# Kernel tuning notes

Hardware: AMD Instinct MI355X
Metric: run time of the kernel (lower is better)

Reference implementation:

```python
import jax, jax.numpy as jnp
import numpy as np

SCALE = 0.08838834764831845  # 1/sqrt(128)


def setup_inputs() -> dict:
    key = jax.random.key(0)
    k1, k2, k3, k4, k5 = jax.random.split(key, 5)
    B, H, KVH, D = 32, 32, 8, 128
    NUM_BLOCKS, BLOCK_SIZE, MAX_BLOCKS = 1200, 128, 32
    return {
        "query": jax.random.normal(k1, (B, H, D), dtype=jnp.float32),
        "key_cache": jax.random.normal(k2, (NUM_BLOCKS, BLOCK_SIZE, KVH, D), dtype=jnp.float32),
        "value_cache": jax.random.normal(k3, (NUM_BLOCKS, BLOCK_SIZE, KVH, D), dtype=jnp.float32),
        "block_tables": jax.random.randint(k4, (B, MAX_BLOCKS), 0, NUM_BLOCKS, dtype=jnp.int32),
        "context_lens": jax.random.randint(k5, (B,), 1, MAX_BLOCKS * BLOCK_SIZE, dtype=jnp.int32),
    }


def reference(query, key_cache, value_cache, block_tables, context_lens):
    # Paged attention v1 decode (single query token per sequence, GQA).
    B, H, D = query.shape
    NB = block_tables.shape[1]
    BS, KVH = key_cache.shape[1], key_cache.shape[2]
    G = H // KVH  # queries per kv head
    S = NB * BS   # padded kv length

    # Gather cache blocks per sequence: [B, NB, BS, KVH, D] -> [B, KVH, S, D]
    keys = key_cache[block_tables].transpose(0, 3, 1, 2, 4).reshape(B, KVH, S, D)
    vals = value_cache[block_tables].transpose(0, 3, 1, 2, 4).reshape(B, KVH, S, D)

    q = (query * SCALE).reshape(B, KVH, G, D)
    scores = jnp.einsum('bkgd,bksd->bkgs', q, keys)  # [B, KVH, G, S]

    # Mask positions beyond context length with dtype-min (as masked_fill in torch).
    pos = jnp.arange(S, dtype=jnp.int32)
    invalid = pos[None, :] >= context_lens[:, None]  # [B, S]
    scores = jnp.where(invalid[:, None, None, :], jnp.finfo(scores.dtype).min, scores)

    w = jax.nn.softmax(scores, axis=-1)
    out = jnp.einsum('bkgs,bksd->bkgd', w, vals).reshape(B, H, D)
    return out
```

## Files before the change

### kernel.cpp

```cpp
#include <hip/hip_runtime.h>

#define SCALE 0.08838834764831845f

constexpr int B_    = 32;
constexpr int H_    = 32;
constexpr int KVH_  = 8;
constexpr int G_    = 4;
constexpr int D_    = 128;
constexpr int BS_   = 128;
constexpr int MAXB_ = 32;
constexpr int NSPLIT = 8;
constexpr int CHUNK  = 4096 / NSPLIT;
constexpr int NBLK_PER_CHUNK = CHUNK / BS_;

__global__ __launch_bounds__(256) void attn_partial(
    const float* __restrict__ q,
    const float* __restrict__ kc,
    const float* __restrict__ vc,
    const int*   __restrict__ bt,
    const int*   __restrict__ ctxl,
    float*       __restrict__ part_o,
    float*       __restrict__ part_ml)
{
    const int bid   = blockIdx.x;
    const int split = bid & (NSPLIT - 1);
    const int kv    = (bid >> 3) & (KVH_ - 1);
    const int b     = bid >> 6;
    const int tid   = threadIdx.x;

    const int ctx   = ctxl[b];
    const int start = split * CHUNK;
    int clen = ctx - start;
    if (clen > CHUNK) clen = CHUNK;

    const int mlbase = ((b * KVH_ + kv) * NSPLIT + split) * G_ * 2;
    if (clen <= 0) {
        if (tid < G_) {
            part_ml[mlbase + tid * 2 + 0] = -__builtin_inff();
            part_ml[mlbase + tid * 2 + 1] = 0.f;
        }
        return;
    }

    __shared__ float q_s[G_ * D_];
    __shared__ float logit[G_][CHUNK];
    __shared__ float red[8 * G_ * D_];
    __shared__ int   blk_s[NBLK_PER_CHUNK];
    __shared__ float red_m[4][G_];
    __shared__ float red_l[4][G_];

    for (int i = tid; i < G_ * D_; i += 256) {
        int g = i >> 7, d = i & (D_ - 1);
        q_s[i] = q[((size_t)b * H_ + kv * G_ + g) * D_ + d] * SCALE;
    }
    if (tid < NBLK_PER_CHUNK)
        blk_s[tid] = bt[b * MAXB_ + split * NBLK_PER_CHUNK + tid];
    __syncthreads();

    {
        const int ln16 = tid & 15;
        const int cl   = tid >> 4;

        float4 qr[G_][2];
#pragma unroll
        for (int g = 0; g < G_; g++) {
            const float4* qp = (const float4*)(q_s + g * D_);
            qr[g][0] = qp[ln16];
            qr[g][1] = qp[ln16 + 16];
        }

#pragma unroll 2
        for (int p = cl; p < clen; p += 16) {
            const int blk = blk_s[p >> 7];
            const int off = p & (BS_ - 1);
            const float4* kp =
                (const float4*)(kc + ((((size_t)blk * BS_ + off) * KVH_ + kv) << 7))
                + ln16;
            float4 ka = kp[0];
            float4 kb = kp[16];
            float s[G_];
#pragma unroll
            for (int g = 0; g < G_; g++) {
                s[g] = ka.x * qr[g][0].x + ka.y * qr[g][0].y +
                       ka.z * qr[g][0].z + ka.w * qr[g][0].w +
                       kb.x * qr[g][1].x + kb.y * qr[g][1].y +
                       kb.z * qr[g][1].z + kb.w * qr[g][1].w;
            }
#pragma unroll
            for (int m = 8; m >= 1; m >>= 1) {
#pragma unroll
                for (int g = 0; g < G_; g++)
                    s[g] += __shfl_xor(s[g], m, 64);
            }
            if (ln16 == 0) {
#pragma unroll
                for (int g = 0; g < G_; g++) logit[g][p] = s[g];
            }
        }
    }
    __syncthreads();

    float ml[G_];
#pragma unroll
    for (int g = 0; g < G_; g++) ml[g] = -__builtin_inff();
    for (int i = tid; i < clen; i += 256) {
#pragma unroll
        for (int g = 0; g < G_; g++) ml[g] = fmaxf(ml[g], logit[g][i]);
    }
#pragma unroll
    for (int m = 32; m >= 1; m >>= 1) {
#pragma unroll
        for (int g = 0; g < G_; g++)
            ml[g] = fmaxf(ml[g], __shfl_xor(ml[g], m, 64));
    }
    if ((tid & 63) == 0) {
#pragma unroll
        for (int g = 0; g < G_; g++) red_m[tid >> 6][g] = ml[g];
    }
    __syncthreads();
    float M[G_];
#pragma unroll
    for (int g = 0; g < G_; g++)
        M[g] = fmaxf(fmaxf(red_m[0][g], red_m[1][g]),
                     fmaxf(red_m[2][g], red_m[3][g]));

    float ll[G_] = {0.f, 0.f, 0.f, 0.f};
    for (int i = tid; i < clen; i += 256) {
#pragma unroll
        for (int g = 0; g < G_; g++) {
            float pv = __expf(logit[g][i] - M[g]);
            logit[g][i] = pv;
            ll[g] += pv;
        }
    }
#pragma unroll
    for (int m = 32; m >= 1; m >>= 1) {
#pragma unroll
        for (int g = 0; g < G_; g++) ll[g] += __shfl_xor(ll[g], m, 64);
    }
    if ((tid & 63) == 0) {
#pragma unroll
        for (int g = 0; g < G_; g++) red_l[tid >> 6][g] = ll[g];
    }
    __syncthreads();
    float L[G_];
#pragma unroll
    for (int g = 0; g < G_; g++)
        L[g] = red_l[0][g] + red_l[1][g] + red_l[2][g] + red_l[3][g];

    const int lane = tid & 31;
    const int grp  = tid >> 5;

    float4 acc[G_] = {};
#pragma unroll 2
    for (int i = grp; i < clen; i += 8) {
        const int blk = blk_s[i >> 7];
        const int off = i & (BS_ - 1);
        const float4* vp =
            (const float4*)(vc + ((((size_t)blk * BS_ + off) * KVH_ + kv) << 7));
        float4 v4 = vp[lane];
#pragma unroll
        for (int g = 0; g < G_; g++) {
            float w = logit[g][i];
            acc[g].x += w * v4.x; acc[g].y += w * v4.y;
            acc[g].z += w * v4.z; acc[g].w += w * v4.w;
        }
    }
    float4* red4 = (float4*)red;
#pragma unroll
    for (int g = 0; g < G_; g++)
        red4[(grp * G_ + g) * 32 + lane] = acc[g];
    __syncthreads();

    const size_t obase = (size_t)((b * KVH_ + kv) * NSPLIT + split) * (G_ * D_);
    for (int e = tid; e < G_ * D_; e += 256) {
        float sum = 0.f;
#pragma unroll
        for (int p = 0; p < 8; p++) sum += red[p * (G_ * D_) + e];
        part_o[obase + e] = sum;
    }
    if (tid == 0) {
#pragma unroll
        for (int g = 0; g < G_; g++) {
            part_ml[mlbase + g * 2 + 0] = M[g];
            part_ml[mlbase + g * 2 + 1] = L[g];
        }
    }
}

__global__ __launch_bounds__(256) void attn_reduce(
    const float* __restrict__ part_o,
    const float* __restrict__ part_ml,
    float*       __restrict__ out)
{
    const int bid = blockIdx.x;
    const int tid = threadIdx.x;

    __shared__ float sc[G_][NSPLIT];
    __shared__ float Ls[G_];

    if (tid < G_) {
        float m = -__builtin_inff();
        float lv[NSPLIT], mv[NSPLIT];
#pragma unroll
        for (int s = 0; s < NSPLIT; s++) {
            mv[s] = part_ml[((size_t)bid * NSPLIT + s) * G_ * 2 + tid * 2 + 0];
            lv[s] = part_ml[((size_t)bid * NSPLIT + s) * G_ * 2 + tid * 2 + 1];
            if (lv[s] > 0.f) m = fmaxf(m, mv[s]);
        }
        float L = 0.f;
#pragma unroll
        for (int s = 0; s < NSPLIT; s++) {
            float f = (lv[s] > 0.f) ? __expf(mv[s] - m) : 0.f;
            sc[tid][s] = f;
            L += f * lv[s];
        }
        Ls[tid] = L;
    }
    __syncthreads();

    for (int e = tid; e < G_ * D_; e += 256) {
        int g = e >> 7;
        float a = 0.f;
#pragma unroll
        for (int s = 0; s < NSPLIT; s++) {
            float f = sc[g][s];
            if (f != 0.f)
                a += f * part_o[((size_t)bid * NSPLIT + s) * (G_ * D_) + e];
        }
        out[(size_t)bid * (G_ * D_) + e] = a / Ls[g];
    }
}

extern "C" void kernel_launch(void* const* d_in, const int* in_sizes, int n_in,
                              void* d_out, int out_size, void* d_ws, size_t ws_size,
                              hipStream_t stream) {
    const float* q   = (const float*)d_in[0];
    const float* kc  = (const float*)d_in[1];
    const float* vc  = (const float*)d_in[2];
    const int*   bt  = (const int*)d_in[3];
    const int*   ctx = (const int*)d_in[4];
    float* out = (float*)d_out;

    float* part_o  = (float*)d_ws;
    float* part_ml = part_o + (size_t)B_ * KVH_ * NSPLIT * G_ * D_;

    attn_partial<<<B_ * KVH_ * NSPLIT, 256, 0, stream>>>(q, kc, vc, bt, ctx,
                                                         part_o, part_ml);
    attn_reduce<<<B_ * KVH_, 256, 0, stream>>>(part_o, part_ml, out);
}
```

Measured before the change: 1.060 ms.

## Process all KV heads per block over contiguous 64-token chunks with 64 splits

```diff
diff --git a/kernel.cpp b/kernel.cpp
--- a/kernel.cpp
+++ b/kernel.cpp
@@ -9,9 +9,9 @@
 constexpr int D_    = 128;
 constexpr int BS_   = 128;
 constexpr int MAXB_ = 32;
-constexpr int NSPLIT = 8;
+constexpr int NSPLIT = 64;
 constexpr int CHUNK  = 4096 / NSPLIT;
-constexpr int NBLK_PER_CHUNK = CHUNK / BS_;
+constexpr int LPAD   = 36;
 
 __global__ __launch_bounds__(256) void attn_partial(
     const float* __restrict__ q,
@@ -24,168 +24,108 @@
 {
     const int bid   = blockIdx.x;
     const int split = bid & (NSPLIT - 1);
-    const int kv    = (bid >> 3) & (KVH_ - 1);
     const int b     = bid >> 6;
     const int tid   = threadIdx.x;
 
-    const int ctx   = ctxl[b];
-    const int start = split * CHUNK;
-    int clen = ctx - start;
+    const int ctx = ctxl[b];
+    int clen = ctx - split * CHUNK;
     if (clen > CHUNK) clen = CHUNK;
-
-    const int mlbase = ((b * KVH_ + kv) * NSPLIT + split) * G_ * 2;
     if (clen <= 0) {
-        if (tid < G_) {
-            part_ml[mlbase + tid * 2 + 0] = -__builtin_inff();
-            part_ml[mlbase + tid * 2 + 1] = 0.f;
+        if (tid < KVH_ * G_) {
+            const int kv = tid >> 2, g = tid & 3;
+            const size_t mb =
+                ((size_t)(b * KVH_ + kv) * NSPLIT + split) * (G_ * 2) + g * 2;
+            part_ml[mb + 0] = -__builtin_inff();
+            part_ml[mb + 1] = 0.f;
         }
         return;
     }
 
-    __shared__ float q_s[G_ * D_];
-    __shared__ float logit[G_][CHUNK];
-    __shared__ float red[8 * G_ * D_];
-    __shared__ int   blk_s[NBLK_PER_CHUNK];
-    __shared__ float red_m[4][G_];
-    __shared__ float red_l[4][G_];
+    __shared__ __align__(16) float logit2[CHUNK][LPAD];
 
-    for (int i = tid; i < G_ * D_; i += 256) {
-        int g = i >> 7, d = i & (D_ - 1);
-        q_s[i] = q[((size_t)b * H_ + kv * G_ + g) * D_ + d] * SCALE;
+    const int hw  = tid >> 5;
+    const int l32 = tid & 31;
+
+    const int blk  = bt[b * MAXB_ + (split >> 1)];
+    const int poff = (split & 1) * CHUNK;
+    const float* kbase =
+        kc + (((size_t)blk * BS_ + poff) * KVH_ + hw) * D_ + l32 * 4;
+
+    float4 qf[G_];
+#pragma unroll
+    for (int g = 0; g < G_; g++) {
+        qf[g] = *(const float4*)(q + ((size_t)b * H_ + hw * G_ + g) * D_ + l32 * 4);
+        qf[g].x *= SCALE; qf[g].y *= SCALE; qf[g].z *= SCALE; qf[g].w *= SCALE;
     }
-    if (tid < NBLK_PER_CHUNK)
-        blk_s[tid] = bt[b * MAXB_ + split * NBLK_PER_CHUNK + tid];
+
+#pragma unroll 2
+    for (int p = 0; p < clen; ++p) {
+        const float4 k4 = *(const float4*)(kbase + (size_t)p * (KVH_ * D_));
+        float s0 = k4.x*qf[0].x + k4.y*qf[0].y + k4.z*qf[0].z + k4.w*qf[0].w;
+        float s1 = k4.x*qf[1].x + k4.y*qf[1].y + k4.z*qf[1].z + k4.w*qf[1].w;
+        float s2 = k4.x*qf[2].x + k4.y*qf[2].y + k4.z*qf[2].z + k4.w*qf[2].w;
+        float s3 = k4.x*qf[3].x + k4.y*qf[3].y + k4.z*qf[3].z + k4.w*qf[3].w;
+#pragma unroll
+        for (int m = 4; m <= 16; m <<= 1) {
+            s0 += __shfl_xor(s0, m, 64);
+            s1 += __shfl_xor(s1, m, 64);
+            s2 += __shfl_xor(s2, m, 64);
+            s3 += __shfl_xor(s3, m, 64);
+        }
+        const bool o1 = (l32 & 1) != 0, o2 = (l32 & 2) != 0;
+        float a01 = o1 ? s0 : s1;  float r01 = __shfl_xor(a01, 1, 64);
+        float uA  = (o1 ? s1 : s0) + r01;
+        float a23 = o1 ? s2 : s3;  float r23 = __shfl_xor(a23, 1, 64);
+        float uB  = (o1 ? s3 : s2) + r23;
+        float v   = o2 ? uA : uB;  float rv  = __shfl_xor(v, 2, 64);
+        float fin = (o2 ? uB : uA) + rv;
+        if (l32 < 4) logit2[p][hw * G_ + l32] = fin;
+    }
     __syncthreads();
 
     {
-        const int ln16 = tid & 15;
-        const int cl   = tid >> 4;
-
-        float4 qr[G_][2];
+        const int h = tid >> 3, ln8 = tid & 7;
+        float m = -__builtin_inff();
+        for (int i = ln8; i < clen; i += 8) m = fmaxf(m, logit2[i][h]);
 #pragma unroll
-        for (int g = 0; g < G_; g++) {
-            const float4* qp = (const float4*)(q_s + g * D_);
-            qr[g][0] = qp[ln16];
-            qr[g][1] = qp[ln16 + 16];
+        for (int mk = 4; mk >= 1; mk >>= 1)
+            m = fmaxf(m, __shfl_xor(m, mk, 64));
+        float l = 0.f;
+        for (int i = ln8; i < clen; i += 8) {
+            float pv = __expf(logit2[i][h] - m);
+            logit2[i][h] = pv;
+            l += pv;
         }
-
-#pragma unroll 2
-        for (int p = cl; p < clen; p += 16) {
-            const int blk = blk_s[p >> 7];
-            const int off = p & (BS_ - 1);
-            const float4* kp =
-                (const float4*)(kc + ((((size_t)blk * BS_ + off) * KVH_ + kv) << 7))
-                + ln16;
-            float4 ka = kp[0];
-            float4 kb = kp[16];
-            float s[G_];
 #pragma unroll
-            for (int g = 0; g < G_; g++) {
-                s[g] = ka.x * qr[g][0].x + ka.y * qr[g][0].y +
-                       ka.z * qr[g][0].z + ka.w * qr[g][0].w +
-                       kb.x * qr[g][1].x + kb.y * qr[g][1].y +
-                       kb.z * qr[g][1].z + kb.w * qr[g][1].w;
-            }
-#pragma unroll
-            for (int m = 8; m >= 1; m >>= 1) {
-#pragma unroll
-                for (int g = 0; g < G_; g++)
-                    s[g] += __shfl_xor(s[g], m, 64);
-            }
-            if (ln16 == 0) {
-#pragma unroll
-                for (int g = 0; g < G_; g++) logit[g][p] = s[g];
-            }
+        for (int mk = 4; mk >= 1; mk >>= 1) l += __shfl_xor(l, mk, 64);
+        if (ln8 == 0) {
+            const size_t mb =
+                ((size_t)(b * KVH_ + (h >> 2)) * NSPLIT + split) * (G_ * 2) +
+                (h & 3) * 2;
+            part_ml[mb + 0] = m;
+            part_ml[mb + 1] = l;
         }
     }
     __syncthreads();
 
-    float ml[G_];
-#pragma unroll
-    for (int g = 0; g < G_; g++) ml[g] = -__builtin_inff();
-    for (int i = tid; i < clen; i += 256) {
-#pragma unroll
-        for (int g = 0; g < G_; g++) ml[g] = fmaxf(ml[g], logit[g][i]);
+    const float* vbase =
+        vc + (((size_t)blk * BS_ + poff) * KVH_ + hw) * D_ + l32 * 4;
+    float4 a0 = {0,0,0,0}, a1 = {0,0,0,0}, a2 = {0,0,0,0}, a3 = {0,0,0,0};
+#pragma unroll 4
+    for (int p = 0; p < clen; ++p) {
+        const float4 v4 = *(const float4*)(vbase + (size_t)p * (KVH_ * D_));
+        const float4 w4 = *(const float4*)(&logit2[p][hw * G_]);
+        a0.x += w4.x * v4.x; a0.y += w4.x * v4.y; a0.z += w4.x * v4.z; a0.w += w4.x * v4.w;
+        a1.x += w4.y * v4.x; a1.y += w4.y * v4.y; a1.z += w4.y * v4.z; a1.w += w4.y * v4.w;
+        a2.x += w4.z * v4.x; a2.y += w4.z * v4.y; a2.z += w4.z * v4.z; a2.w += w4.z * v4.w;
+        a3.x += w4.w * v4.x; a3.y += w4.w * v4.y; a3.z += w4.w * v4.z; a3.w += w4.w * v4.w;
     }
-#pragma unroll
-    for (int m = 32; m >= 1; m >>= 1) {
-#pragma unroll
-        for (int g = 0; g < G_; g++)
-            ml[g] = fmaxf(ml[g], __shfl_xor(ml[g], m, 64));
-    }
-    if ((tid & 63) == 0) {
-#pragma unroll
-        for (int g = 0; g < G_; g++) red_m[tid >> 6][g] = ml[g];
-    }
-    __syncthreads();
-    float M[G_];
-#pragma unroll
-    for (int g = 0; g < G_; g++)
-        M[g] = fmaxf(fmaxf(red_m[0][g], red_m[1][g]),
-                     fmaxf(red_m[2][g], red_m[3][g]));
-
-    float ll[G_] = {0.f, 0.f, 0.f, 0.f};
-    for (int i = tid; i < clen; i += 256) {
-#pragma unroll
-        for (int g = 0; g < G_; g++) {
-            float pv = __expf(logit[g][i] - M[g]);
-            logit[g][i] = pv;
-            ll[g] += pv;
-        }
-    }
-#pragma unroll
-    for (int m = 32; m >= 1; m >>= 1) {
-#pragma unroll
-        for (int g = 0; g < G_; g++) ll[g] += __shfl_xor(ll[g], m, 64);
-    }
-    if ((tid & 63) == 0) {
-#pragma unroll
-        for (int g = 0; g < G_; g++) red_l[tid >> 6][g] = ll[g];
-    }
-    __syncthreads();
-    float L[G_];
-#pragma unroll
-    for (int g = 0; g < G_; g++)
-        L[g] = red_l[0][g] + red_l[1][g] + red_l[2][g] + red_l[3][g];
-
-    const int lane = tid & 31;
-    const int grp  = tid >> 5;
-
-    float4 acc[G_] = {};
-#pragma unroll 2
-    for (int i = grp; i < clen; i += 8) {
-        const int blk = blk_s[i >> 7];
-        const int off = i & (BS_ - 1);
-        const float4* vp =
-            (const float4*)(vc + ((((size_t)blk * BS_ + off) * KVH_ + kv) << 7));
-        float4 v4 = vp[lane];
-#pragma unroll
-        for (int g = 0; g < G_; g++) {
-            float w = logit[g][i];
-            acc[g].x += w * v4.x; acc[g].y += w * v4.y;
-            acc[g].z += w * v4.z; acc[g].w += w * v4.w;
-        }
-    }
-    float4* red4 = (float4*)red;
-#pragma unroll
-    for (int g = 0; g < G_; g++)
-        red4[(grp * G_ + g) * 32 + lane] = acc[g];
-    __syncthreads();
-
-    const size_t obase = (size_t)((b * KVH_ + kv) * NSPLIT + split) * (G_ * D_);
-    for (int e = tid; e < G_ * D_; e += 256) {
-        float sum = 0.f;
-#pragma unroll
-        for (int p = 0; p < 8; p++) sum += red[p * (G_ * D_) + e];
-        part_o[obase + e] = sum;
-    }
-    if (tid == 0) {
-#pragma unroll
-        for (int g = 0; g < G_; g++) {
-            part_ml[mlbase + g * 2 + 0] = M[g];
-            part_ml[mlbase + g * 2 + 1] = L[g];
-        }
-    }
+    const size_t ob =
+        ((size_t)(b * KVH_ + hw) * NSPLIT + split) * (G_ * D_) + l32 * 4;
+    *(float4*)(part_o + ob + 0 * D_) = a0;
+    *(float4*)(part_o + ob + 1 * D_) = a1;
+    *(float4*)(part_o + ob + 2 * D_) = a2;
+    *(float4*)(part_o + ob + 3 * D_) = a3;
 }
 
 __global__ __launch_bounds__(256) void attn_reduce(
@@ -199,32 +139,30 @@
     __shared__ float sc[G_][NSPLIT];
     __shared__ float Ls[G_];
 
-    if (tid < G_) {
-        float m = -__builtin_inff();
-        float lv[NSPLIT], mv[NSPLIT];
+    {
+        const int g = tid >> 6, s = tid & 63;
+        const size_t base = ((size_t)bid * NSPLIT + s) * (G_ * 2) + g * 2;
+        const float mv = part_ml[base + 0];
+        const float lv = part_ml[base + 1];
+        float key = (lv > 0.f) ? mv : -__builtin_inff();
 #pragma unroll
-        for (int s = 0; s < NSPLIT; s++) {
-            mv[s] = part_ml[((size_t)bid * NSPLIT + s) * G_ * 2 + tid * 2 + 0];
-            lv[s] = part_ml[((size_t)bid * NSPLIT + s) * G_ * 2 + tid * 2 + 1];
-            if (lv[s] > 0.f) m = fmaxf(m, mv[s]);
-        }
-        float L = 0.f;
+        for (int mk = 32; mk >= 1; mk >>= 1)
+            key = fmaxf(key, __shfl_xor(key, mk, 64));
+        const float f = (lv > 0.f) ? __expf(mv - key) : 0.f;
+        sc[g][s] = f;
+        float fl = f * lv;
 #pragma unroll
-        for (int s = 0; s < NSPLIT; s++) {
-            float f = (lv[s] > 0.f) ? __expf(mv[s] - m) : 0.f;
-            sc[tid][s] = f;
-            L += f * lv[s];
-        }
-        Ls[tid] = L;
+        for (int mk = 32; mk >= 1; mk >>= 1) fl += __shfl_xor(fl, mk, 64);
+        if (s == 0) Ls[g] = fl;
     }
     __syncthreads();
 
     for (int e = tid; e < G_ * D_; e += 256) {
-        int g = e >> 7;
+        const int g = e >> 7;
         float a = 0.f;
-#pragma unroll
+#pragma unroll 4
         for (int s = 0; s < NSPLIT; s++) {
-            float f = sc[g][s];
+            const float f = sc[g][s];
             if (f != 0.f)
                 a += f * part_o[((size_t)bid * NSPLIT + s) * (G_ * D_) + e];
         }
@@ -245,7 +183,7 @@
     float* part_o  = (float*)d_ws;
     float* part_ml = part_o + (size_t)B_ * KVH_ * NSPLIT * G_ * D_;
 
-    attn_partial<<<B_ * KVH_ * NSPLIT, 256, 0, stream>>>(q, kc, vc, bt, ctx,
-                                                         part_o, part_ml);
+    attn_partial<<<B_ * NSPLIT, 256, 0, stream>>>(q, kc, vc, bt, ctx,
+                                                  part_o, part_ml);
     attn_reduce<<<B_ * KVH_, 256, 0, stream>>>(part_o, part_ml, out);
 }
```

Measured after the change: 1.067 ms. No clear change (+0.7%).
